# Performance work log

Hardware: AMD Instinct MI355X
Metric: run time of the kernel (lower is better)

The kernel has to match this reference:

```python
import jax, jax.numpy as jnp
import numpy as np

DIM = 768
HEADS = 12
HEAD_DIM = DIM // HEADS


def setup_inputs() -> dict:
    key = jax.random.key(0)
    ks = jax.random.split(key, 5)
    B, N = 2, 2048
    x = jax.random.normal(ks[0], (B, N, DIM), dtype=jnp.float32)
    s = 1.0 / np.sqrt(DIM)
    qkv_w = jax.random.normal(ks[1], (3 * DIM, DIM), dtype=jnp.float32) * s
    qkv_b = jnp.zeros((3 * DIM,), dtype=jnp.float32)
    proj_w = jax.random.normal(ks[2], (DIM, DIM), dtype=jnp.float32) * s
    proj_b = jnp.zeros((DIM,), dtype=jnp.float32)
    return {"x": x, "qkv_w": qkv_w, "qkv_b": qkv_b, "proj_w": proj_w, "proj_b": proj_b}


def reference(x, qkv_w, qkv_b, proj_w, proj_b):
    B, N, C = x.shape
    scale = HEAD_DIM ** -0.5
    qkv = x @ qkv_w.T + qkv_b                      # [B,N,3C]
    qkv = qkv.reshape(B, N, 3, HEADS, HEAD_DIM)
    q = qkv[:, :, 0].transpose(0, 2, 1, 3)         # [B,H,N,D]
    k = qkv[:, :, 1].transpose(0, 2, 1, 3)
    v = qkv[:, :, 2].transpose(0, 2, 1, 3)
    attn = jnp.einsum('bhnd,bhmd->bhnm', q, k) * scale
    attn = jax.nn.softmax(attn, axis=-1)
    out = jnp.einsum('bhnm,bhmd->bhnd', attn, v)   # [B,H,N,D]
    out = out.transpose(0, 2, 1, 3).reshape(B, N, C)
    return out @ proj_w.T + proj_b
```

## Files before the change

kernel.cpp:

```cpp
#include <hip/hip_runtime.h>
#include <hip/hip_bf16.h>

typedef __bf16 bf16x8 __attribute__((ext_vector_type(8)));
typedef float f32x4 __attribute__((ext_vector_type(4)));
typedef float f32x16 __attribute__((ext_vector_type(16)));

#define SEQ   2048
#define NHEAD 12
#define NBH   24
#define QSCALE 0.18033688011112042f

#define CP16(g, l) __builtin_amdgcn_global_load_lds( \
    (const __attribute__((address_space(1))) unsigned int*)(g), \
    (__attribute__((address_space(3))) unsigned int*)(l), 16, 0, 0)

__device__ __forceinline__ unsigned short f2bf(float f) {
  unsigned int u = __builtin_bit_cast(unsigned int, f);
  u += 0x7FFFu + ((u >> 16) & 1u);
  return (unsigned short)(u >> 16);
}
__device__ __forceinline__ unsigned int packbf2_trunc(float lo, float hi) {
  return __builtin_amdgcn_perm(__builtin_bit_cast(unsigned int, hi),
                               __builtin_bit_cast(unsigned int, lo), 0x07060302u);
}

#define NX4  786432
#define NW14 442368
__global__ __launch_bounds__(256) void cvt3_kernel(const float4* __restrict__ x,
                                                   const float4* __restrict__ w1,
                                                   const float4* __restrict__ w2,
                                                   ushort4* __restrict__ xo,
                                                   ushort4* __restrict__ w1o,
                                                   ushort4* __restrict__ w2o) {
  int i = blockIdx.x * 256 + threadIdx.x;
  const float4* s;
  ushort4* d;
  int j = i;
  if (i < NX4)               { s = x;  d = xo; }
  else if (i < NX4 + NW14)   { s = w1; d = w1o; j = i - NX4; }
  else                       { s = w2; d = w2o; j = i - (NX4 + NW14); }
  float4 v = s[j];
  ushort4 r;
  r.x = f2bf(v.x); r.y = f2bf(v.y); r.z = f2bf(v.z); r.w = f2bf(v.w);
  d[j] = r;
}

template <int BM, int BN, int MODE>
__global__ __launch_bounds__(256) void gemm_kernel(const unsigned short* __restrict__ X,
                                                   const unsigned short* __restrict__ W,
                                                   const float* __restrict__ bias,
                                                   unsigned short* __restrict__ Qb,
                                                   unsigned short* __restrict__ Kb,
                                                   unsigned short* __restrict__ Vtb,
                                                   float* __restrict__ Out) {
  constexpr int K = 768, BK = 64;
  constexpr int WM = BM / 2, WN = BN / 2;
  constexpr int MT = WM / 16, NT = WN / 16;
  __shared__ __align__(16) unsigned short Xs[BM * BK];
  __shared__ __align__(16) unsigned short Ws[BN * BK];

  const int tid = threadIdx.x;
  const int w = tid >> 6, lane = tid & 63, quad = lane >> 4, m16 = lane & 15;
  const int wm = w & 1, wn = w >> 1;
  const int row0 = blockIdx.y * BM, col0 = blockIdx.x * BN;

  f32x4 acc[MT][NT];
#pragma unroll
  for (int mt = 0; mt < MT; ++mt)
#pragma unroll
    for (int nt = 0; nt < NT; ++nt) acc[mt][nt] = (f32x4){0.f, 0.f, 0.f, 0.f};

  for (int k0 = 0; k0 < K; k0 += BK) {
    __syncthreads();
#pragma unroll
    for (int j = 0; j < BM / 32; ++j) {
      int e = tid + 256 * j, r = e >> 3, c8 = e & 7;
      CP16(X + (size_t)(row0 + r) * 768 + k0 + ((c8 ^ (r & 7)) << 3), Xs + e * 8);
    }
#pragma unroll
    for (int j = 0; j < BN / 32; ++j) {
      int e = tid + 256 * j, r = e >> 3, c8 = e & 7;
      CP16(W + (size_t)(col0 + r) * 768 + k0 + ((c8 ^ (r & 7)) << 3), Ws + e * 8);
    }
    __syncthreads();
#pragma unroll
    for (int ks = 0; ks < 2; ++ks) {
      const int sw = ((quad + 4 * ks) ^ (m16 & 7)) << 3;
      bf16x8 a[MT], b[NT];
#pragma unroll
      for (int mt = 0; mt < MT; ++mt)
        a[mt] = *(const bf16x8*)(Xs + (wm * WM + mt * 16 + m16) * BK + sw);
#pragma unroll
      for (int nt = 0; nt < NT; ++nt)
        b[nt] = *(const bf16x8*)(Ws + (wn * WN + nt * 16 + m16) * BK + sw);
#pragma unroll
      for (int mt = 0; mt < MT; ++mt)
#pragma unroll
        for (int nt = 0; nt < NT; ++nt)
          acc[mt][nt] = __builtin_amdgcn_mfma_f32_16x16x32_bf16(a[mt], b[nt], acc[mt][nt], 0, 0, 0);
    }
  }

#pragma unroll
  for (int mt = 0; mt < MT; ++mt) {
#pragma unroll
    for (int nt = 0; nt < NT; ++nt) {
      const int m0 = row0 + wm * WM + mt * 16 + quad * 4;
      const int c = col0 + wn * WN + nt * 16 + m16;
      const float bia = bias[c];
      f32x4 v = acc[mt][nt];
      if constexpr (MODE == 0) {
        const int bidx = m0 >> 11, ns = m0 & 2047;
        if (c < 1536) {
          unsigned short* dst;
          float sc;
          int cc;
          if (c < 768) { cc = c; dst = Qb; sc = QSCALE; }
          else         { cc = c - 768; dst = Kb; sc = 1.0f; }
          const int h = cc >> 6, d = cc & 63;
          unsigned short* p = dst + ((size_t)(bidx * NHEAD + h) * SEQ + ns) * 64 + d;
          p[0]   = f2bf((v[0] + bia) * sc);
          p[64]  = f2bf((v[1] + bia) * sc);
          p[128] = f2bf((v[2] + bia) * sc);
          p[192] = f2bf((v[3] + bia) * sc);
        } else {
          const int cc = c - 1536, h = cc >> 6, d = cc & 63;
          const int ns2 = (ns & ~12) | ((ns & 4) << 1) | ((ns & 8) >> 1);
          ushort4 pk;
          pk.x = f2bf(v[0] + bia); pk.y = f2bf(v[1] + bia);
          pk.z = f2bf(v[2] + bia); pk.w = f2bf(v[3] + bia);
          *(ushort4*)(Vtb + ((size_t)(bidx * NHEAD + h) * 64 + d) * SEQ + ns2) = pk;
        }
      } else {
        float* o = Out + (size_t)m0 * 768 + c;
        o[0]       = v[0] + bia;
        o[768]     = v[1] + bia;
        o[2 * 768] = v[2] + bia;
        o[3 * 768] = v[3] + bia;
      }
    }
  }
}

__global__ __launch_bounds__(128) void attn_kernel(const unsigned short* __restrict__ Qb,
                                                   const unsigned short* __restrict__ Kb,
                                                   const unsigned short* __restrict__ Vtb,
                                                   unsigned short* __restrict__ Ab) {
  __shared__ __align__(16) unsigned short Ks[2][64 * 64];
  __shared__ __align__(16) unsigned short Vts[2][64 * 64];

  const int tid = threadIdx.x;
  const int w = tid >> 6, lane = tid & 63, hi = lane >> 5, l32 = lane & 31;
  const int bh = blockIdx.x % NBH, qt = blockIdx.x / NBH;
  const int bb = bh / NHEAD, h = bh % NHEAD;
  const int q0 = qt * 64 + w * 32;

  const unsigned short* Qp = Qb + (size_t)bh * SEQ * 64;
  const unsigned short* Kp = Kb + (size_t)bh * SEQ * 64;
  const unsigned short* Vp = Vtb + (size_t)bh * 64 * SEQ;

  bf16x8 qf[4];
#pragma unroll
  for (int dc = 0; dc < 4; ++dc)
    qf[dc] = *(const bf16x8*)(Qp + (size_t)(q0 + l32) * 64 + dc * 16 + hi * 8);

#pragma unroll
  for (int j = 0; j < 4; ++j) {
    int e = tid + 128 * j, r = e >> 3, c8 = e & 7;
    CP16(Kp + (size_t)r * 64 + ((c8 ^ (r & 7)) << 3), &Ks[0][e * 8]);
    CP16(Vp + (size_t)r * SEQ + ((c8 ^ (r & 7)) << 3), &Vts[0][e * 8]);
  }

  f32x16 o[2] = {};
  float m_i = -3.0e38f, l_i = 0.f;

  for (int kt = 0; kt < 32; ++kt) {
    const int cur = kt & 1;
    __syncthreads();

    const unsigned short* Kc = Ks[cur];
    const unsigned short* Vc = Vts[cur];
    bf16x8 kf[2][4], vf[2][4];
#pragma unroll
    for (int t32 = 0; t32 < 2; ++t32)
#pragma unroll
      for (int dc = 0; dc < 4; ++dc)
        kf[t32][dc] = *(const bf16x8*)(Kc + (t32 * 32 + l32) * 64 + ((((dc << 1) | hi) ^ (l32 & 7)) << 3));
#pragma unroll
    for (int dt = 0; dt < 2; ++dt)
#pragma unroll
      for (int cc = 0; cc < 4; ++cc)
        vf[dt][cc] = *(const bf16x8*)(Vc + (dt * 32 + l32) * 64 + ((((cc << 1) | hi) ^ (l32 & 7)) << 3));

    if (kt < 31) {
      const int kn = kt + 1, nb = 1 - cur;
#pragma unroll
      for (int j = 0; j < 4; ++j) {
        int e = tid + 128 * j, r = e >> 3, c8 = e & 7;
        CP16(Kp + (size_t)(kn * 64 + r) * 64 + ((c8 ^ (r & 7)) << 3), &Ks[nb][e * 8]);
        CP16(Vp + (size_t)r * SEQ + kn * 64 + ((c8 ^ (r & 7)) << 3), &Vts[nb][e * 8]);
      }
    }

    f32x16 st[2];
#pragma unroll
    for (int t32 = 0; t32 < 2; ++t32) {
      f32x16 s = {};
#pragma unroll
      for (int dc = 0; dc < 4; ++dc)
        s = __builtin_amdgcn_mfma_f32_32x32x16_bf16(kf[t32][dc], qf[dc], s, 0, 0, 0);
      st[t32] = s;
    }

    float tmax = st[0][0];
#pragma unroll
    for (int t32 = 0; t32 < 2; ++t32)
#pragma unroll
      for (int e = 0; e < 16; ++e) tmax = fmaxf(tmax, st[t32][e]);
    tmax = fmaxf(tmax, __shfl_xor(tmax, 32));
    const float mnew = fmaxf(m_i, tmax);
    const float alpha = __builtin_amdgcn_exp2f(m_i - mnew);
    float ssum = 0.f;
    unsigned int pf[2][8];
#pragma unroll
    for (int t32 = 0; t32 < 2; ++t32) {
      float pv[16];
#pragma unroll
      for (int e = 0; e < 16; ++e) { pv[e] = __builtin_amdgcn_exp2f(st[t32][e] - mnew); ssum += pv[e]; }
#pragma unroll
      for (int e2 = 0; e2 < 8; ++e2)
        pf[t32][e2] = packbf2_trunc(pv[2 * e2], pv[2 * e2 + 1]);
    }
    ssum += __shfl_xor(ssum, 32);
    l_i = l_i * alpha + ssum;
    m_i = mnew;
    o[0] *= alpha;
    o[1] *= alpha;

#pragma unroll
    for (int t32 = 0; t32 < 2; ++t32) {
#pragma unroll
      for (int hh = 0; hh < 2; ++hh) {
        bf16x8 pfrag = __builtin_bit_cast(bf16x8,
            make_uint4(pf[t32][hh * 4], pf[t32][hh * 4 + 1], pf[t32][hh * 4 + 2], pf[t32][hh * 4 + 3]));
        const int cc = 2 * t32 + hh;
#pragma unroll
        for (int dt = 0; dt < 2; ++dt)
          o[dt] = __builtin_amdgcn_mfma_f32_32x32x16_bf16(vf[dt][cc], pfrag, o[dt], 0, 0, 0);
      }
    }
  }

  const float rl = __builtin_amdgcn_rcpf(l_i);
  unsigned short* base = Ab + ((size_t)bb * SEQ + q0 + l32) * 768 + h * 64;
#pragma unroll
  for (int dt = 0; dt < 2; ++dt) {
#pragma unroll
    for (int run = 0; run < 4; ++run) {
      ushort4 pk;
      pk.x = f2bf(o[dt][run * 4 + 0] * rl);
      pk.y = f2bf(o[dt][run * 4 + 1] * rl);
      pk.z = f2bf(o[dt][run * 4 + 2] * rl);
      pk.w = f2bf(o[dt][run * 4 + 3] * rl);
      *(ushort4*)(base + dt * 32 + run * 8 + hi * 4) = pk;
    }
  }
}

extern "C" void kernel_launch(void* const* d_in, const int* in_sizes, int n_in,
                              void* d_out, int out_size, void* d_ws, size_t ws_size,
                              hipStream_t stream) {
  const float* x      = (const float*)d_in[0];
  const float* qkv_w  = (const float*)d_in[1];
  const float* qkv_b  = (const float*)d_in[2];
  const float* proj_w = (const float*)d_in[3];
  const float* proj_b = (const float*)d_in[4];
  float* out = (float*)d_out;

  unsigned short* xb  = (unsigned short*)d_ws;
  unsigned short* wqb = xb + 3145728;
  unsigned short* wpb = wqb + 1769472;
  unsigned short* Qb  = wpb + 589824;
  unsigned short* Kb  = Qb + 3145728;
  unsigned short* Vtb = Kb + 3145728;
  unsigned short* Ab  = Vtb + 3145728;

  cvt3_kernel<<<5376, 256, 0, stream>>>((const float4*)x, (const float4*)qkv_w, (const float4*)proj_w,
                                        (ushort4*)xb, (ushort4*)wqb, (ushort4*)wpb);
  gemm_kernel<128, 96, 0><<<dim3(24, 32), 256, 0, stream>>>(xb, wqb, qkv_b, Qb, Kb, Vtb, nullptr);
  attn_kernel<<<768, 128, 0, stream>>>(Qb, Kb, Vtb, Ab);
  gemm_kernel<64, 96, 1><<<dim3(8, 64), 256, 0, stream>>>(Ab, wpb, proj_b, nullptr, nullptr, nullptr, out);
}
```

Measured before the change: 169.5 us.

## Tune attention kernel: precomputed LDS addresses, tree reductions, setprio around MFMA

```diff
diff --git a/kernel.cpp b/kernel.cpp
--- a/kernel.cpp
+++ b/kernel.cpp
@@ -22,6 +22,13 @@
 __device__ __forceinline__ unsigned int packbf2_trunc(float lo, float hi) {
   return __builtin_amdgcn_perm(__builtin_bit_cast(unsigned int, hi),
                                __builtin_bit_cast(unsigned int, lo), 0x07060302u);
+}
+__device__ __forceinline__ float vmax16(const f32x16& s) {
+  float a = fmaxf(fmaxf(s[0], s[1]), fmaxf(s[2], s[3]));
+  float b = fmaxf(fmaxf(s[4], s[5]), fmaxf(s[6], s[7]));
+  float c = fmaxf(fmaxf(s[8], s[9]), fmaxf(s[10], s[11]));
+  float d = fmaxf(fmaxf(s[12], s[13]), fmaxf(s[14], s[15]));
+  return fmaxf(fmaxf(a, b), fmaxf(c, d));
 }
 
 #define NX4  786432
@@ -142,12 +149,11 @@
   }
 }
 
-__global__ __launch_bounds__(128) void attn_kernel(const unsigned short* __restrict__ Qb,
-                                                   const unsigned short* __restrict__ Kb,
-                                                   const unsigned short* __restrict__ Vtb,
-                                                   unsigned short* __restrict__ Ab) {
-  __shared__ __align__(16) unsigned short Ks[2][64 * 64];
-  __shared__ __align__(16) unsigned short Vts[2][64 * 64];
+__global__ __launch_bounds__(128, 1) void attn_kernel(const unsigned short* __restrict__ Qb,
+                                                      const unsigned short* __restrict__ Kb,
+                                                      const unsigned short* __restrict__ Vtb,
+                                                      unsigned short* __restrict__ Ab) {
+  __shared__ __align__(16) unsigned short S[4][64 * 64];
 
   const int tid = threadIdx.x;
   const int w = tid >> 6, lane = tid & 63, hi = lane >> 5, l32 = lane & 31;
@@ -164,44 +170,61 @@
   for (int dc = 0; dc < 4; ++dc)
     qf[dc] = *(const bf16x8*)(Qp + (size_t)(q0 + l32) * 64 + dc * 16 + hi * 8);
 
+  const unsigned short* dsb[2][4];
+#pragma unroll
+  for (int t32 = 0; t32 < 2; ++t32)
+#pragma unroll
+    for (int c = 0; c < 4; ++c)
+      dsb[t32][c] = &S[0][(t32 * 32 + l32) * 64 + ((((c << 1) | hi) ^ (l32 & 7)) << 3)];
+
+  int koff[4], voff[4];
 #pragma unroll
   for (int j = 0; j < 4; ++j) {
-    int e = tid + 128 * j, r = e >> 3, c8 = e & 7;
-    CP16(Kp + (size_t)r * 64 + ((c8 ^ (r & 7)) << 3), &Ks[0][e * 8]);
-    CP16(Vp + (size_t)r * SEQ + ((c8 ^ (r & 7)) << 3), &Vts[0][e * 8]);
+    const int e = tid + 128 * j, r = e >> 3, sw = ((e & 7) ^ (r & 7)) << 3;
+    koff[j] = r * 64 + sw;
+    voff[j] = r * SEQ + sw;
+  }
+  const int edst = tid * 8;
+
+#pragma unroll
+  for (int j = 0; j < 4; ++j) {
+    CP16(Kp + koff[j], &S[0][edst + 1024 * j]);
+    CP16(Vp + voff[j], &S[2][edst + 1024 * j]);
   }
 
   f32x16 o[2] = {};
   float m_i = -3.0e38f, l_i = 0.f;
-
+  const unsigned short* Kt = Kp + 4096;
+  const unsigned short* Vt = Vp + 64;
+
+#pragma unroll 2
   for (int kt = 0; kt < 32; ++kt) {
     const int cur = kt & 1;
     __syncthreads();
 
-    const unsigned short* Kc = Ks[cur];
-    const unsigned short* Vc = Vts[cur];
     bf16x8 kf[2][4], vf[2][4];
 #pragma unroll
     for (int t32 = 0; t32 < 2; ++t32)
 #pragma unroll
-      for (int dc = 0; dc < 4; ++dc)
-        kf[t32][dc] = *(const bf16x8*)(Kc + (t32 * 32 + l32) * 64 + ((((dc << 1) | hi) ^ (l32 & 7)) << 3));
+      for (int c = 0; c < 4; ++c)
+        kf[t32][c] = *(const bf16x8*)(dsb[t32][c] + cur * 4096);
 #pragma unroll
     for (int dt = 0; dt < 2; ++dt)
 #pragma unroll
-      for (int cc = 0; cc < 4; ++cc)
-        vf[dt][cc] = *(const bf16x8*)(Vc + (dt * 32 + l32) * 64 + ((((cc << 1) | hi) ^ (l32 & 7)) << 3));
+      for (int c = 0; c < 4; ++c)
+        vf[dt][c] = *(const bf16x8*)(dsb[dt][c] + 8192 + cur * 4096);
 
     if (kt < 31) {
-      const int kn = kt + 1, nb = 1 - cur;
 #pragma unroll
       for (int j = 0; j < 4; ++j) {
-        int e = tid + 128 * j, r = e >> 3, c8 = e & 7;
-        CP16(Kp + (size_t)(kn * 64 + r) * 64 + ((c8 ^ (r & 7)) << 3), &Ks[nb][e * 8]);
-        CP16(Vp + (size_t)r * SEQ + kn * 64 + ((c8 ^ (r & 7)) << 3), &Vts[nb][e * 8]);
+        CP16(Kt + koff[j], &S[1 - cur][edst + 1024 * j]);
+        CP16(Vt + voff[j], &S[3 - cur][edst + 1024 * j]);
       }
     }
-
+    Kt += 4096;
+    Vt += 64;
+
+    __builtin_amdgcn_s_setprio(1);
     f32x16 st[2];
 #pragma unroll
     for (int t32 = 0; t32 < 2; ++t32) {
@@ -211,32 +234,36 @@
         s = __builtin_amdgcn_mfma_f32_32x32x16_bf16(kf[t32][dc], qf[dc], s, 0, 0, 0);
       st[t32] = s;
     }
-
-    float tmax = st[0][0];
-#pragma unroll
-    for (int t32 = 0; t32 < 2; ++t32)
-#pragma unroll
-      for (int e = 0; e < 16; ++e) tmax = fmaxf(tmax, st[t32][e]);
+    __builtin_amdgcn_s_setprio(0);
+
+    float tmax = fmaxf(vmax16(st[0]), vmax16(st[1]));
     tmax = fmaxf(tmax, __shfl_xor(tmax, 32));
     const float mnew = fmaxf(m_i, tmax);
     const float alpha = __builtin_amdgcn_exp2f(m_i - mnew);
-    float ssum = 0.f;
     unsigned int pf[2][8];
+    float ts[2];
 #pragma unroll
     for (int t32 = 0; t32 < 2; ++t32) {
       float pv[16];
 #pragma unroll
-      for (int e = 0; e < 16; ++e) { pv[e] = __builtin_amdgcn_exp2f(st[t32][e] - mnew); ssum += pv[e]; }
+      for (int e = 0; e < 16; ++e) pv[e] = __builtin_amdgcn_exp2f(st[t32][e] - mnew);
 #pragma unroll
       for (int e2 = 0; e2 < 8; ++e2)
         pf[t32][e2] = packbf2_trunc(pv[2 * e2], pv[2 * e2 + 1]);
-    }
+      const float a = (pv[0] + pv[1]) + (pv[2] + pv[3]);
+      const float b = (pv[4] + pv[5]) + (pv[6] + pv[7]);
+      const float c = (pv[8] + pv[9]) + (pv[10] + pv[11]);
+      const float d = (pv[12] + pv[13]) + (pv[14] + pv[15]);
+      ts[t32] = (a + b) + (c + d);
+    }
+    float ssum = ts[0] + ts[1];
     ssum += __shfl_xor(ssum, 32);
     l_i = l_i * alpha + ssum;
     m_i = mnew;
     o[0] *= alpha;
     o[1] *= alpha;
 
+    __builtin_amdgcn_s_setprio(1);
 #pragma unroll
     for (int t32 = 0; t32 < 2; ++t32) {
 #pragma unroll
@@ -249,6 +276,7 @@
           o[dt] = __builtin_amdgcn_mfma_f32_32x32x16_bf16(vf[dt][cc], pfrag, o[dt], 0, 0, 0);
       }
     }
+    __builtin_amdgcn_s_setprio(0);
   }
 
   const float rl = __builtin_amdgcn_rcpf(l_i);
```

After: 171.7 us. Within noise of the previous version (+1.3%).
